# Kernel tuning notes

Measured on AMD Instinct MI355X. Metric: run time of the kernel, lower is better.

Reference implementation:

```python
import jax, jax.numpy as jnp
import numpy as np

T, D, H, E, K = 2048, 1024, 512, 16, 4  # tokens, d_model, d_expert, n_experts, top_k


def setup_inputs() -> dict:
    key = jax.random.key(0)
    ks = jax.random.split(key, 5)
    x = jax.random.normal(ks[0], (T, D), dtype=jnp.float32)
    centroids = jax.random.normal(ks[1], (E, D), dtype=jnp.float32) * 0.006
    bias = jnp.zeros((E,), dtype=jnp.float32)  # router bias buffer (aux_loss=True adds it)
    w_gate = jax.random.normal(ks[2], (E, D, H), dtype=jnp.float32) * (1.0 / np.sqrt(D))
    w_up = jax.random.normal(ks[3], (E, D, H), dtype=jnp.float32) * (1.0 / np.sqrt(D))
    w_down = jax.random.normal(ks[4], (E, H, D), dtype=jnp.float32) * (1.0 / np.sqrt(H))
    scale = jnp.ones((1,), dtype=jnp.float32) * 0.1
    return {"x": x, "centroids": centroids, "bias": bias,
            "w_gate": w_gate, "w_up": w_up, "w_down": w_down, "scale": scale}


def reference(x, centroids, bias, w_gate, w_up, w_down, scale):
    n_exp = w_gate.shape[0]
    # Router: sigmoid(x @ C^T + bias), top-k, gates normalized to sum 1.
    logits = x @ centroids.T + bias                      # [T, E]
    scores = jax.nn.sigmoid(logits)
    gates, idx = jax.lax.top_k(scores, K)                # [T, K]
    gates = gates / jnp.clip(gates.sum(axis=-1, keepdims=True), 1e-9)
    # Scatter gates into dense per-expert combine weights [T, E]
    # (top-k indices are unique per token, so one_hot-sum == scatter-set).
    combine = jnp.sum(jax.nn.one_hot(idx, n_exp, dtype=x.dtype) * gates[..., None], axis=1)
    # SwiGLU per expert, weighted by combine gates (zero gate => zero contribution,
    # identical math to the per-expert gather/index_add_ loop).
    h = jax.nn.silu(jnp.einsum('td,edh->teh', x, w_gate)) * jnp.einsum('td,edh->teh', x, w_up)
    h = h * combine[:, :, None]                          # [T, E, H]
    out = jnp.einsum('teh,ehd->td', h, w_down) * scale   # [T, D]
    return out
```

## Files before the change

### kernel.cpp

```cpp
#include <hip/hip_runtime.h>
#include <hip/hip_bf16.h>

#define T_TOK 2048
#define DMODEL 1024
#define HEXP 512
#define NEXP 16
#define TOPK 4
#define CAP 2048

typedef __attribute__((ext_vector_type(4))) float f32x4;
typedef __attribute__((ext_vector_type(8))) short short8;
typedef __attribute__((ext_vector_type(4))) unsigned short ush4;
typedef __attribute__((ext_vector_type(8))) unsigned short ush8;
typedef __attribute__((ext_vector_type(4))) int i32x4;

static __device__ __forceinline__ unsigned short f2bf(float f) {
  union { float f; unsigned int u; } v; v.f = f;
  unsigned int r = v.u + 0x7FFFu + ((v.u >> 16) & 1u);
  return (unsigned short)(r >> 16);
}

static __device__ __forceinline__ void gl16(const unsigned short* g, unsigned short* l) {
  __builtin_amdgcn_global_load_lds(
      (const __attribute__((address_space(1))) unsigned int*)g,
      (__attribute__((address_space(3))) unsigned int*)l, 16, 0, 0);
}

#define SWZ128(r, kb) (((r) << 7) + ((((kb) >> 3) ^ ((r) & 15)) << 3))

__global__ __launch_bounds__(256) void tcast(const float* __restrict__ in,
                                             unsigned short* __restrict__ out,
                                             int R, int C) {
  __shared__ unsigned short lds[64][68];
  int e = blockIdx.z;
  in  += (size_t)e * R * C;
  out += (size_t)e * R * C;
  int r0 = blockIdx.x * 64, c0 = blockIdx.y * 64;
  int tid = (int)threadIdx.x;
  int rr = tid >> 4;
  int cc = (tid & 15) * 4;
#pragma unroll
  for (int i = 0; i < 4; i++) {
    int row = rr + i * 16;
    f32x4 v = *(const f32x4*)(in + (size_t)(r0 + row) * C + c0 + cc);
    ush4 b = { f2bf(v[0]), f2bf(v[1]), f2bf(v[2]), f2bf(v[3]) };
    *(ush4*)&lds[row][cc] = b;
  }
  __syncthreads();
#pragma unroll
  for (int j = 0; j < 4; j++) {
    int orow = rr + j * 16;
    ush4 b = { lds[cc + 0][orow], lds[cc + 1][orow], lds[cc + 2][orow], lds[cc + 3][orow] };
    *(ush4*)(out + (size_t)(c0 + orow) * R + r0 + cc) = b;
  }
}

__global__ __launch_bounds__(256) void router(const float* __restrict__ x,
                                              const float* __restrict__ cen,
                                              const float* __restrict__ bias,
                                              unsigned short* __restrict__ xbf,
                                              int* __restrict__ selIdx,
                                              float* __restrict__ selGate) {
  int tid = (int)threadIdx.x;
  int lane = tid & 63, wid = tid >> 6;
  int t = blockIdx.x * 4 + wid;
  const float* xr = x + (size_t)t * DMODEL;
  f32x4 xv[4];
#pragma unroll
  for (int i = 0; i < 4; i++) xv[i] = *(const f32x4*)(xr + i * 256 + lane * 4);
  unsigned short* xb = xbf + (size_t)t * DMODEL;
#pragma unroll
  for (int i = 0; i < 4; i++) {
    ush4 b = { f2bf(xv[i][0]), f2bf(xv[i][1]), f2bf(xv[i][2]), f2bf(xv[i][3]) };
    *(ush4*)(xb + i * 256 + lane * 4) = b;
  }
  float p[16];
#pragma unroll
  for (int e = 0; e < NEXP; e++) p[e] = 0.f;
#pragma unroll
  for (int e = 0; e < NEXP; e++) {
    const float* ce = cen + (size_t)e * DMODEL;
#pragma unroll
    for (int i = 0; i < 4; i++) {
      f32x4 cv = *(const f32x4*)(ce + i * 256 + lane * 4);
#pragma unroll
      for (int j = 0; j < 4; j++) p[e] = fmaf(xv[i][j], cv[j], p[e]);
    }
  }
#pragma unroll
  for (int o = 32; o >= 1; o >>= 1) {
#pragma unroll
    for (int e = 0; e < NEXP; e++) p[e] += __shfl_xor(p[e], o);
  }
  float s[16];
#pragma unroll
  for (int e = 0; e < NEXP; e++) s[e] = 1.f / (1.f + expf(-(p[e] + bias[e])));
  int sel[4]; float val[4]; float gsum = 0.f;
#pragma unroll
  for (int k = 0; k < 4; k++) {
    float best = -1e30f; int bi = 0;
#pragma unroll
    for (int e = 0; e < NEXP; e++) {
      if (s[e] > best) { best = s[e]; bi = e; }
    }
    sel[k] = bi; val[k] = best; gsum += best;
#pragma unroll
    for (int e = 0; e < NEXP; e++) if (e == bi) s[e] = -1e30f;
  }
  float inv = 1.f / fmaxf(gsum, 1e-9f);
  if (lane == 0) {
    i32x4 si = { sel[0], sel[1], sel[2], sel[3] };
    f32x4 sg = { val[0] * inv, val[1] * inv, val[2] * inv, val[3] * inv };
    *(i32x4*)&selIdx[t * 4] = si;
    *(f32x4*)&selGate[t * 4] = sg;
  }
}

__global__ __launch_bounds__(256) void buildlists(const int* __restrict__ selIdx,
                                                  const float* __restrict__ selGate,
                                                  int* __restrict__ cnt,
                                                  int* __restrict__ listTok,
                                                  float* __restrict__ listGate,
                                                  int* __restrict__ listSlot) {
  int e = blockIdx.x;
  int tid = (int)threadIdx.x, lane = tid & 63, w = tid >> 6;
  int i0 = tid * 32;
  int vals[32];
#pragma unroll
  for (int j = 0; j < 8; j++)
    *(i32x4*)&vals[j * 4] = *(const i32x4*)&selIdx[i0 + j * 4];
  int mycount = 0;
#pragma unroll
  for (int j = 0; j < 32; j++) mycount += (vals[j] == e) ? 1 : 0;
  int s = mycount;
#pragma unroll
  for (int o = 1; o < 64; o <<= 1) {
    int n = __shfl_up(s, o);
    if (lane >= o) s += n;
  }
  __shared__ int wtot[4];
  if (lane == 63) wtot[w] = s;
  __syncthreads();
  int wbase = 0;
#pragma unroll
  for (int j = 0; j < 4; j++) wbase += (j < w) ? wtot[j] : 0;
  int pos = wbase + s - mycount;
#pragma unroll
  for (int j = 0; j < 32; j++) {
    if (vals[j] == e) {
      int i = i0 + j;
      listTok[e * CAP + pos]  = i >> 2;
      listGate[e * CAP + pos] = selGate[i];
      listSlot[e * CAP + pos] = i;
      pos++;
    }
  }
  if (tid == 255) cnt[e] = pos;
}

__global__ __launch_bounds__(256) void ffn1(const unsigned short* __restrict__ xbf,
                                            const unsigned short* __restrict__ wgT,
                                            const unsigned short* __restrict__ wuT,
                                            const int* __restrict__ cnt,
                                            const int* __restrict__ listTok,
                                            const float* __restrict__ listGate,
                                            unsigned short* __restrict__ hbuf) {
  int b = (int)blockIdx.x;
  int xcd = b & 7, slot = b >> 3;
  int e = xcd + 8 * (slot >> 7);
  int tile = slot & 127;
  int my = tile >> 3;
  int nx = tile & 7;
  int c = cnt[e];
  int m0 = my * 128;
  if (m0 >= c) return;
  int n0 = nx * 64;
  __shared__ unsigned short sA[16384];
  __shared__ unsigned short sG[8192];
  __shared__ unsigned short sU[8192];
  __shared__ int sTok[128];
  __shared__ float sGate[128];
  int tid = (int)threadIdx.x;
  if (tid < 128) {
    int r = m0 + tid;
    sTok[tid]  = (r < c) ? listTok[e * CAP + r] : listTok[e * CAP];
    sGate[tid] = (r < c) ? listGate[e * CAP + r] : 0.f;
  }
  __syncthreads();
  int lane = tid & 63, wid = tid >> 6;
  int wr = wid >> 1, wc = wid & 1;
  const unsigned short* wg = wgT + ((size_t)e * HEXP + n0) * DMODEL;
  const unsigned short* wu = wuT + ((size_t)e * HEXP + n0) * DMODEL;
  int rl = lane >> 4;
  int lg = lane & 15;
  const unsigned short* pA[8];
#pragma unroll
  for (int i = 0; i < 8; i++) {
    int lr = wid * 32 + i * 4 + rl;
    int cg = lg ^ ((i * 4 + rl) & 15);
    pA[i] = xbf + (size_t)sTok[lr] * DMODEL + cg * 8;
  }
  const unsigned short* pG[4];
  const unsigned short* pU[4];
#pragma unroll
  for (int j = 0; j < 4; j++) {
    int lr = wid * 16 + j * 4 + rl;
    int cg = lg ^ ((j * 4 + rl) & 15);
    pG[j] = wg + (size_t)lr * DMODEL + cg * 8;
    pU[j] = wu + (size_t)lr * DMODEL + cg * 8;
  }
  f32x4 ag[4][2] = {{{0,0,0,0},{0,0,0,0}},{{0,0,0,0},{0,0,0,0}},
                    {{0,0,0,0},{0,0,0,0}},{{0,0,0,0},{0,0,0,0}}};
  f32x4 au[4][2] = {{{0,0,0,0},{0,0,0,0}},{{0,0,0,0},{0,0,0,0}},
                    {{0,0,0,0},{0,0,0,0}},{{0,0,0,0},{0,0,0,0}}};
#pragma unroll 1
  for (int k0 = 0; k0 < DMODEL; k0 += 128) {
    __syncthreads();
#pragma unroll
    for (int i = 0; i < 8; i++)
      gl16(pA[i] + k0, sA + (wid * 32 + i * 4) * 128);
#pragma unroll
    for (int j = 0; j < 4; j++) {
      gl16(pG[j] + k0, sG + (wid * 16 + j * 4) * 128);
      gl16(pU[j] + k0, sU + (wid * 16 + j * 4) * 128);
    }
    __syncthreads();
#pragma unroll
    for (int kk = 0; kk < 4; kk++) {
      int kb = (kk << 5) + (rl << 3);
      short8 a[4], g[2], u[2];
#pragma unroll
      for (int m = 0; m < 4; m++)
        a[m] = *(const short8*)&sA[SWZ128((wr << 6) + lg + m * 16, kb)];
#pragma unroll
      for (int n = 0; n < 2; n++) {
        g[n] = *(const short8*)&sG[SWZ128((wc << 5) + lg + n * 16, kb)];
        u[n] = *(const short8*)&sU[SWZ128((wc << 5) + lg + n * 16, kb)];
      }
#pragma unroll
      for (int m = 0; m < 4; m++) {
#pragma unroll
        for (int n = 0; n < 2; n++) {
          ag[m][n] = __builtin_amdgcn_mfma_f32_16x16x32_bf16(a[m], g[n], ag[m][n], 0, 0, 0);
          au[m][n] = __builtin_amdgcn_mfma_f32_16x16x32_bf16(a[m], u[n], au[m][n], 0, 0, 0);
        }
      }
    }
  }
  int rlo = (lane >> 4) << 2;
  int cl = lane & 15;
#pragma unroll
  for (int m = 0; m < 4; m++) {
#pragma unroll
    for (int r = 0; r < 4; r++) {
      int row = (wr << 6) + m * 16 + rlo + r;
      int grow = m0 + row;
      if (grow < c) {
        float gwt = sGate[row];
#pragma unroll
        for (int n = 0; n < 2; n++) {
          int col = n0 + (wc << 5) + n * 16 + cl;
          float g = ag[m][n][r];
          float u = au[m][n][r];
          float sig = 1.f / (1.f + __expf(-g));
          float h = g * sig * u * gwt;
          hbuf[((size_t)e * CAP + grow) * HEXP + col] = f2bf(h);
        }
      }
    }
  }
}

__global__ __launch_bounds__(256) void ffn2(const unsigned short* __restrict__ hbuf,
                                            const unsigned short* __restrict__ wdT,
                                            const int* __restrict__ cnt,
                                            const int* __restrict__ listSlot,
                                            float* __restrict__ y) {
  int b = (int)blockIdx.x;
  int xcd = b & 7, slot = b >> 3;
  int e = xcd + 8 * (slot >> 7);
  int tile = slot & 127;
  int my = tile >> 3;
  int nx = tile & 7;
  int c = cnt[e];
  int m0 = my * 128;
  if (m0 >= c) return;
  int n0 = nx * 128;
  __shared__ unsigned short sA[16384];
  __shared__ unsigned short sB[16384];
  __shared__ int sSlot[128];
  int tid = (int)threadIdx.x;
  if (tid < 128) {
    int r = m0 + tid;
    sSlot[tid] = (r < c) ? listSlot[e * CAP + r] : 0;
  }
  __syncthreads();
  int lane = tid & 63, wid = tid >> 6;
  int wr = wid >> 1, wc = wid & 1;
  const unsigned short* ha = hbuf + ((size_t)e * CAP + m0) * HEXP;
  const unsigned short* wd = wdT + ((size_t)e * DMODEL + n0) * HEXP;
  int rl = lane >> 4;
  int lg = lane & 15;
  const unsigned short* pA[8];
  const unsigned short* pB[8];
#pragma unroll
  for (int i = 0; i < 8; i++) {
    int lr = wid * 32 + i * 4 + rl;
    int cg = lg ^ ((i * 4 + rl) & 15);
    pA[i] = ha + (size_t)lr * HEXP + cg * 8;
    pB[i] = wd + (size_t)lr * HEXP + cg * 8;
  }
  f32x4 acc[4][4];
#pragma unroll
  for (int m = 0; m < 4; m++)
#pragma unroll
    for (int n = 0; n < 4; n++) acc[m][n] = f32x4{0, 0, 0, 0};
#pragma unroll 1
  for (int k0 = 0; k0 < HEXP; k0 += 128) {
    __syncthreads();
#pragma unroll
    for (int i = 0; i < 8; i++) {
      gl16(pA[i] + k0, sA + (wid * 32 + i * 4) * 128);
      gl16(pB[i] + k0, sB + (wid * 32 + i * 4) * 128);
    }
    __syncthreads();
#pragma unroll
    for (int kk = 0; kk < 4; kk++) {
      int kb = (kk << 5) + (rl << 3);
      short8 a[4], bb[4];
#pragma unroll
      for (int m = 0; m < 4; m++)
        a[m] = *(const short8*)&sA[SWZ128((wr << 6) + lg + m * 16, kb)];
#pragma unroll
      for (int n = 0; n < 4; n++)
        bb[n] = *(const short8*)&sB[SWZ128((wc << 6) + lg + n * 16, kb)];
#pragma unroll
      for (int m = 0; m < 4; m++) {
#pragma unroll
        for (int n = 0; n < 4; n++)
          acc[m][n] = __builtin_amdgcn_mfma_f32_16x16x32_bf16(a[m], bb[n], acc[m][n], 0, 0, 0);
      }
    }
  }
  int rlo = (lane >> 4) << 2;
  int cl = lane & 15;
#pragma unroll
  for (int m = 0; m < 4; m++) {
#pragma unroll
    for (int r = 0; r < 4; r++) {
      int row = (wr << 6) + m * 16 + rlo + r;
      int grow = m0 + row;
      if (grow < c) {
        int slot2 = sSlot[row];
#pragma unroll
        for (int n = 0; n < 4; n++) {
          int col = n0 + (wc << 6) + n * 16 + cl;
          y[(size_t)slot2 * DMODEL + col] = acc[m][n][r];
        }
      }
    }
  }
}

__global__ __launch_bounds__(256) void reducek(const float* __restrict__ y,
                                               const float* __restrict__ scale,
                                               float* __restrict__ out) {
  int i = blockIdx.x * 256 + (int)threadIdx.x;
  int t = i >> 8;
  int d = (i & 255) << 2;
  const float* yb = y + (size_t)t * 4 * DMODEL + d;
  f32x4 s = *(const f32x4*)(yb);
  s += *(const f32x4*)(yb + DMODEL);
  s += *(const f32x4*)(yb + 2 * DMODEL);
  s += *(const f32x4*)(yb + 3 * DMODEL);
  float sc = scale[0];
  s *= sc;
  *(f32x4*)(out + (size_t)t * DMODEL + d) = s;
}

extern "C" void kernel_launch(void* const* d_in, const int* in_sizes, int n_in,
                              void* d_out, int out_size, void* d_ws, size_t ws_size,
                              hipStream_t stream) {
  const float* x      = (const float*)d_in[0];
  const float* cen    = (const float*)d_in[1];
  const float* bias   = (const float*)d_in[2];
  const float* w_gate = (const float*)d_in[3];
  const float* w_up   = (const float*)d_in[4];
  const float* w_down = (const float*)d_in[5];
  const float* scale  = (const float*)d_in[6];
  float* out = (float*)d_out;

  char* ws = (char*)d_ws;
  unsigned short* xbf  = (unsigned short*)(ws);
  unsigned short* wgT  = (unsigned short*)(ws + 4194304);
  unsigned short* wuT  = (unsigned short*)(ws + 20971520);
  unsigned short* wdT  = (unsigned short*)(ws + 37748736);
  unsigned short* hbuf = (unsigned short*)(ws + 54525952);
  float*          y    = (float*)(ws + 88080384);
  int*            cnt  = (int*)(ws + 121634816);
  int*        listTok  = (int*)(ws + 121635072);
  float*     listGate  = (float*)(ws + 121766144);
  int*       listSlot  = (int*)(ws + 121897216);
  int*         selIdx  = (int*)(ws + 122028288);
  float*      selGate  = (float*)(ws + 122061056);

  tcast<<<dim3(16, 8, 16), 256, 0, stream>>>(w_gate, wgT, 1024, 512);
  tcast<<<dim3(16, 8, 16), 256, 0, stream>>>(w_up,   wuT, 1024, 512);
  tcast<<<dim3(8, 16, 16), 256, 0, stream>>>(w_down, wdT, 512, 1024);
  router<<<dim3(512), 256, 0, stream>>>(x, cen, bias, xbf, selIdx, selGate);
  buildlists<<<dim3(16), 256, 0, stream>>>(selIdx, selGate, cnt, listTok, listGate, listSlot);
  ffn1<<<dim3(2048), 256, 0, stream>>>(xbf, wgT, wuT, cnt, listTok, listGate, hbuf);
  ffn2<<<dim3(2048), 256, 0, stream>>>(hbuf, wdT, cnt, listSlot, y);
  reducek<<<dim3(2048), 256, 0, stream>>>(y, scale, out);
}
```

Measured before the change: 115.5 us.

## Use 8 waves per block in expert GEMMs and merge weight transpose launches

The two expert GEMM kernels now run 512 threads per block, with 8 waves arranged 4x2, so each wave owns half as many M rows and keeps fewer accumulators. Each wave issues half as many async global-to-LDS loads. The three weight transpose-cast launches are merged into one 6144-block launch that picks its tensor from the block index, cutting launch overhead. In exchange, more waves share each barrier and each wave does less MFMA work per LDS read of the B fragments.

```diff
diff --git a/kernel.cpp b/kernel.cpp
--- a/kernel.cpp
+++ b/kernel.cpp
@@ -28,14 +28,25 @@
 
 #define SWZ128(r, kb) (((r) << 7) + ((((kb) >> 3) ^ ((r) & 15)) << 3))
 
-__global__ __launch_bounds__(256) void tcast(const float* __restrict__ in,
-                                             unsigned short* __restrict__ out,
-                                             int R, int C) {
+__global__ __launch_bounds__(256) void tcast_all(const float* __restrict__ w_gate,
+                                                 const float* __restrict__ w_up,
+                                                 const float* __restrict__ w_down,
+                                                 unsigned short* __restrict__ wgT,
+                                                 unsigned short* __restrict__ wuT,
+                                                 unsigned short* __restrict__ wdT) {
   __shared__ unsigned short lds[64][68];
-  int e = blockIdx.z;
+  int b = (int)blockIdx.x;
+  int sel = b >> 11, bb = b & 2047;
+  const float* in; unsigned short* out; int R, C, rx, cy, e;
+  if (sel == 0)      { in = w_gate; out = wgT; R = 1024; C = 512;
+                       rx = bb & 15; cy = (bb >> 4) & 7; e = bb >> 7; }
+  else if (sel == 1) { in = w_up;   out = wuT; R = 1024; C = 512;
+                       rx = bb & 15; cy = (bb >> 4) & 7; e = bb >> 7; }
+  else               { in = w_down; out = wdT; R = 512;  C = 1024;
+                       rx = bb & 7;  cy = (bb >> 3) & 15; e = bb >> 7; }
   in  += (size_t)e * R * C;
   out += (size_t)e * R * C;
-  int r0 = blockIdx.x * 64, c0 = blockIdx.y * 64;
+  int r0 = rx * 64, c0 = cy * 64;
   int tid = (int)threadIdx.x;
   int rr = tid >> 4;
   int cc = (tid & 15) * 4;
@@ -43,15 +54,15 @@
   for (int i = 0; i < 4; i++) {
     int row = rr + i * 16;
     f32x4 v = *(const f32x4*)(in + (size_t)(r0 + row) * C + c0 + cc);
-    ush4 b = { f2bf(v[0]), f2bf(v[1]), f2bf(v[2]), f2bf(v[3]) };
-    *(ush4*)&lds[row][cc] = b;
+    ush4 bo = { f2bf(v[0]), f2bf(v[1]), f2bf(v[2]), f2bf(v[3]) };
+    *(ush4*)&lds[row][cc] = bo;
   }
   __syncthreads();
 #pragma unroll
   for (int j = 0; j < 4; j++) {
     int orow = rr + j * 16;
-    ush4 b = { lds[cc + 0][orow], lds[cc + 1][orow], lds[cc + 2][orow], lds[cc + 3][orow] };
-    *(ush4*)(out + (size_t)(c0 + orow) * R + r0 + cc) = b;
+    ush4 bo = { lds[cc + 0][orow], lds[cc + 1][orow], lds[cc + 2][orow], lds[cc + 3][orow] };
+    *(ush4*)(out + (size_t)(c0 + orow) * R + r0 + cc) = bo;
   }
 }
 
@@ -158,7 +169,7 @@
   if (tid == 255) cnt[e] = pos;
 }
 
-__global__ __launch_bounds__(256) void ffn1(const unsigned short* __restrict__ xbf,
+__global__ __launch_bounds__(512) void ffn1(const unsigned short* __restrict__ xbf,
                                             const unsigned short* __restrict__ wgT,
                                             const unsigned short* __restrict__ wuT,
                                             const int* __restrict__ cnt,
@@ -193,52 +204,50 @@
   const unsigned short* wu = wuT + ((size_t)e * HEXP + n0) * DMODEL;
   int rl = lane >> 4;
   int lg = lane & 15;
-  const unsigned short* pA[8];
-#pragma unroll
-  for (int i = 0; i < 8; i++) {
-    int lr = wid * 32 + i * 4 + rl;
-    int cg = lg ^ ((i * 4 + rl) & 15);
+  const unsigned short* pA[4];
+#pragma unroll
+  for (int i = 0; i < 4; i++) {
+    int lr = wid * 16 + i * 4 + rl;
+    int cg = lg ^ (lr & 15);
     pA[i] = xbf + (size_t)sTok[lr] * DMODEL + cg * 8;
   }
-  const unsigned short* pG[4];
-  const unsigned short* pU[4];
-#pragma unroll
-  for (int j = 0; j < 4; j++) {
-    int lr = wid * 16 + j * 4 + rl;
-    int cg = lg ^ ((j * 4 + rl) & 15);
+  const unsigned short* pG[2];
+  const unsigned short* pU[2];
+#pragma unroll
+  for (int j = 0; j < 2; j++) {
+    int lr = wid * 8 + j * 4 + rl;
+    int cg = lg ^ (lr & 15);
     pG[j] = wg + (size_t)lr * DMODEL + cg * 8;
     pU[j] = wu + (size_t)lr * DMODEL + cg * 8;
   }
-  f32x4 ag[4][2] = {{{0,0,0,0},{0,0,0,0}},{{0,0,0,0},{0,0,0,0}},
-                    {{0,0,0,0},{0,0,0,0}},{{0,0,0,0},{0,0,0,0}}};
-  f32x4 au[4][2] = {{{0,0,0,0},{0,0,0,0}},{{0,0,0,0},{0,0,0,0}},
-                    {{0,0,0,0},{0,0,0,0}},{{0,0,0,0},{0,0,0,0}}};
+  f32x4 ag[2][2] = {{{0,0,0,0},{0,0,0,0}},{{0,0,0,0},{0,0,0,0}}};
+  f32x4 au[2][2] = {{{0,0,0,0},{0,0,0,0}},{{0,0,0,0},{0,0,0,0}}};
 #pragma unroll 1
   for (int k0 = 0; k0 < DMODEL; k0 += 128) {
     __syncthreads();
 #pragma unroll
-    for (int i = 0; i < 8; i++)
-      gl16(pA[i] + k0, sA + (wid * 32 + i * 4) * 128);
-#pragma unroll
-    for (int j = 0; j < 4; j++) {
-      gl16(pG[j] + k0, sG + (wid * 16 + j * 4) * 128);
-      gl16(pU[j] + k0, sU + (wid * 16 + j * 4) * 128);
+    for (int i = 0; i < 4; i++)
+      gl16(pA[i] + k0, sA + (wid * 16 + i * 4) * 128);
+#pragma unroll
+    for (int j = 0; j < 2; j++) {
+      gl16(pG[j] + k0, sG + (wid * 8 + j * 4) * 128);
+      gl16(pU[j] + k0, sU + (wid * 8 + j * 4) * 128);
     }
     __syncthreads();
 #pragma unroll
     for (int kk = 0; kk < 4; kk++) {
       int kb = (kk << 5) + (rl << 3);
-      short8 a[4], g[2], u[2];
-#pragma unroll
-      for (int m = 0; m < 4; m++)
-        a[m] = *(const short8*)&sA[SWZ128((wr << 6) + lg + m * 16, kb)];
+      short8 a[2], g[2], u[2];
+#pragma unroll
+      for (int m = 0; m < 2; m++)
+        a[m] = *(const short8*)&sA[SWZ128((wr << 5) + lg + m * 16, kb)];
 #pragma unroll
       for (int n = 0; n < 2; n++) {
         g[n] = *(const short8*)&sG[SWZ128((wc << 5) + lg + n * 16, kb)];
         u[n] = *(const short8*)&sU[SWZ128((wc << 5) + lg + n * 16, kb)];
       }
 #pragma unroll
-      for (int m = 0; m < 4; m++) {
+      for (int m = 0; m < 2; m++) {
 #pragma unroll
         for (int n = 0; n < 2; n++) {
           ag[m][n] = __builtin_amdgcn_mfma_f32_16x16x32_bf16(a[m], g[n], ag[m][n], 0, 0, 0);
@@ -250,10 +259,10 @@
   int rlo = (lane >> 4) << 2;
   int cl = lane & 15;
 #pragma unroll
-  for (int m = 0; m < 4; m++) {
+  for (int m = 0; m < 2; m++) {
 #pragma unroll
     for (int r = 0; r < 4; r++) {
-      int row = (wr << 6) + m * 16 + rlo + r;
+      int row = (wr << 5) + m * 16 + rlo + r;
       int grow = m0 + row;
       if (grow < c) {
         float gwt = sGate[row];
@@ -271,7 +280,7 @@
   }
 }
 
-__global__ __launch_bounds__(256) void ffn2(const unsigned short* __restrict__ hbuf,
+__global__ __launch_bounds__(512) void ffn2(const unsigned short* __restrict__ hbuf,
                                             const unsigned short* __restrict__ wdT,
                                             const int* __restrict__ cnt,
                                             const int* __restrict__ listSlot,
@@ -301,41 +310,41 @@
   const unsigned short* wd = wdT + ((size_t)e * DMODEL + n0) * HEXP;
   int rl = lane >> 4;
   int lg = lane & 15;
-  const unsigned short* pA[8];
-  const unsigned short* pB[8];
-#pragma unroll
-  for (int i = 0; i < 8; i++) {
-    int lr = wid * 32 + i * 4 + rl;
-    int cg = lg ^ ((i * 4 + rl) & 15);
+  const unsigned short* pA[4];
+  const unsigned short* pB[4];
+#pragma unroll
+  for (int i = 0; i < 4; i++) {
+    int lr = wid * 16 + i * 4 + rl;
+    int cg = lg ^ (lr & 15);
     pA[i] = ha + (size_t)lr * HEXP + cg * 8;
     pB[i] = wd + (size_t)lr * HEXP + cg * 8;
   }
-  f32x4 acc[4][4];
-#pragma unroll
-  for (int m = 0; m < 4; m++)
+  f32x4 acc[2][4];
+#pragma unroll
+  for (int m = 0; m < 2; m++)
 #pragma unroll
     for (int n = 0; n < 4; n++) acc[m][n] = f32x4{0, 0, 0, 0};
 #pragma unroll 1
   for (int k0 = 0; k0 < HEXP; k0 += 128) {
     __syncthreads();
 #pragma unroll
-    for (int i = 0; i < 8; i++) {
-      gl16(pA[i] + k0, sA + (wid * 32 + i * 4) * 128);
-      gl16(pB[i] + k0, sB + (wid * 32 + i * 4) * 128);
+    for (int i = 0; i < 4; i++) {
+      gl16(pA[i] + k0, sA + (wid * 16 + i * 4) * 128);
+      gl16(pB[i] + k0, sB + (wid * 16 + i * 4) * 128);
     }
     __syncthreads();
 #pragma unroll
     for (int kk = 0; kk < 4; kk++) {
       int kb = (kk << 5) + (rl << 3);
-      short8 a[4], bb[4];
-#pragma unroll
-      for (int m = 0; m < 4; m++)
-        a[m] = *(const short8*)&sA[SWZ128((wr << 6) + lg + m * 16, kb)];
+      short8 a[2], bb[4];
+#pragma unroll
+      for (int m = 0; m < 2; m++)
+        a[m] = *(const short8*)&sA[SWZ128((wr << 5) + lg + m * 16, kb)];
 #pragma unroll
       for (int n = 0; n < 4; n++)
         bb[n] = *(const short8*)&sB[SWZ128((wc << 6) + lg + n * 16, kb)];
 #pragma unroll
-      for (int m = 0; m < 4; m++) {
+      for (int m = 0; m < 2; m++) {
 #pragma unroll
         for (int n = 0; n < 4; n++)
           acc[m][n] = __builtin_amdgcn_mfma_f32_16x16x32_bf16(a[m], bb[n], acc[m][n], 0, 0, 0);
@@ -345,10 +354,10 @@
   int rlo = (lane >> 4) << 2;
   int cl = lane & 15;
 #pragma unroll
-  for (int m = 0; m < 4; m++) {
+  for (int m = 0; m < 2; m++) {
 #pragma unroll
     for (int r = 0; r < 4; r++) {
-      int row = (wr << 6) + m * 16 + rlo + r;
+      int row = (wr << 5) + m * 16 + rlo + r;
       int grow = m0 + row;
       if (grow < c) {
         int slot2 = sSlot[row];
@@ -404,12 +413,10 @@
   int*         selIdx  = (int*)(ws + 122028288);
   float*      selGate  = (float*)(ws + 122061056);
 
-  tcast<<<dim3(16, 8, 16), 256, 0, stream>>>(w_gate, wgT, 1024, 512);
-  tcast<<<dim3(16, 8, 16), 256, 0, stream>>>(w_up,   wuT, 1024, 512);
-  tcast<<<dim3(8, 16, 16), 256, 0, stream>>>(w_down, wdT, 512, 1024);
+  tcast_all<<<dim3(6144), 256, 0, stream>>>(w_gate, w_up, w_down, wgT, wuT, wdT);
   router<<<dim3(512), 256, 0, stream>>>(x, cen, bias, xbf, selIdx, selGate);
   buildlists<<<dim3(16), 256, 0, stream>>>(selIdx, selGate, cnt, listTok, listGate, listSlot);
-  ffn1<<<dim3(2048), 256, 0, stream>>>(xbf, wgT, wuT, cnt, listTok, listGate, hbuf);
-  ffn2<<<dim3(2048), 256, 0, stream>>>(hbuf, wdT, cnt, listSlot, y);
+  ffn1<<<dim3(2048), 512, 0, stream>>>(xbf, wgT, wuT, cnt, listTok, listGate, hbuf);
+  ffn2<<<dim3(2048), 512, 0, stream>>>(hbuf, wdT, cnt, listSlot, y);
   reducek<<<dim3(2048), 256, 0, stream>>>(y, scale, out);
 }
```

Result: faster. 108.5 us (-6.1%).
